# Kernel tuning notes

Hardware: AMD Instinct MI355X
Metric: run time of the kernel (lower is better)

## Reference

```python
import jax, jax.numpy as jnp
import numpy as np

N_NATIVE = 4_000_000
N_EDGES = 500_001  # -> 500_000 wl_centers
MAX_P = 15
TWO_PI = 2 * 3.1415926654  # constant as written in the torch source


def setup_inputs() -> dict:
    key = jax.random.key(0)
    k1, k2 = jax.random.split(key)

    # static wavelength grids (numpy, computed once)
    wl_native = np.linspace(9999.0, 10501.0, N_NATIVE)
    wl_bin_edges = np.linspace(10000.0, 10500.0, N_EDGES)

    # ragged segment labels: which data bin each native point falls into
    labels_np = np.searchsorted(wl_bin_edges, wl_native)  # values in [0, N_EDGES]
    num_segments = N_EDGES + 1
    counts_np = np.bincount(labels_np, minlength=num_segments).astype(np.float32)
    counts_np = np.maximum(counts_np, 1.0)  # all segments occupied by construction

    # polynomial design matrix over normalized bin centers
    wl_centers = 0.5 * (wl_bin_edges[1:] + wl_bin_edges[:-1])
    median_wl = np.median(wl_centers)
    bandwidth = wl_bin_edges[-1] + wl_bin_edges[0]
    wl_normed = (wl_centers - median_wl) / bandwidth
    design_np = wl_normed[:, None] ** np.arange(1, MAX_P + 1)[None, :]  # [500000, 15]

    kernel_grid_np = np.arange(-4.5, 4.51, 0.01)  # 901 taps

    return {
        "high_res_model": jax.random.uniform(k1, (N_NATIVE,), dtype=jnp.float32),
        "ln_sigma": jnp.asarray(-2.8134, dtype=jnp.float32),
        "weight": 0.01 * jax.random.normal(k2, (1, MAX_P), dtype=jnp.float32),
        "bias": jnp.ones((1,), dtype=jnp.float32),
        "kernel_grid": jnp.asarray(kernel_grid_np, dtype=jnp.float32),
        "design_matrix": jnp.asarray(design_np, dtype=jnp.float32),
        "labels": jnp.asarray(labels_np, dtype=jnp.int32),
        "counts": jnp.asarray(counts_np, dtype=jnp.float32),
    }


def reference(high_res_model, ln_sigma, weight, bias, kernel_grid, design_matrix, labels, counts):
    # --- instrumental_broaden: Gaussian conv1d, padding='same' ---
    sigma = 0.01 + jnp.exp(ln_sigma)
    gauss = (1.0 / (sigma * jnp.sqrt(jnp.asarray(TWO_PI, dtype=sigma.dtype)))) \
            * jnp.exp(-0.5 * kernel_grid ** 2 / sigma ** 2) * 0.01  # [901]
    # torch conv1d is cross-correlation; flip kernel for jnp.convolve (symmetric anyway)
    convolved = jnp.convolve(high_res_model, gauss[::-1], mode="same")  # [N_NATIVE]

    # --- resample_to_data: segment mean over ragged label groups ---
    num_segments = counts.shape[0]
    seg_sum = jax.ops.segment_sum(convolved, labels, num_segments=num_segments)
    seg_mean = seg_sum / counts
    resampled = jnp.clip(seg_mean, 0.0, 1.0)[1:-1]  # drop under/overflow bins -> [500000]

    # --- warped_continuum: linear model over polynomial design matrix ---
    continuum = design_matrix @ weight[0] + bias[0]  # [500000]

    return resampled * continuum
```

## Files before the change

### kernel.cpp

```cpp
#include <hip/hip_runtime.h>

#define BLOCK 256
#define SEGS  224
#define DN    2976
#define CVP   2112
#define SG_N  920
#define GTHR  1e-4f
#define NITF  14
#define NL4F  528

__device__ __forceinline__ double vnat(int i, double h, int N) {
    if (i == N - 1) return 10501.0;
    return __dadd_rn(__dmul_rn((double)i, h), 9999.0);
}

__device__ __forceinline__ int seg_start(int e, double h, double q, int N) {
    double E = (e >= 500000) ? 10500.0
                             : __dadd_rn(__dmul_rn((double)e, q), 10000.0);
    double g = (E - 9999.0) / h;
    int i = (int)g - 2;
    if (i < 0) i = 0;
    if (i > N) i = N;
    while (i < N && vnat(i, h, N) <= E) ++i;
    while (i > 0 && vnat(i - 1, h, N) > E) --i;
    return i;
}

__device__ __forceinline__ float continuum(int o, const float* __restrict__ wt,
                                           float bias0) {
    double eo  = 10000.0 + (double)o * 0.001;
    double eo1 = 10000.0 + (double)(o + 1) * 0.001;
    double ci  = 0.5 * (eo + eo1);
    double cA  = 0.5 * ((10000.0 + 249999.0 * 0.001) + (10000.0 + 250000.0 * 0.001));
    double cB  = 0.5 * ((10000.0 + 250000.0 * 0.001) + (10000.0 + 250001.0 * 0.001));
    double med = 0.5 * (cA + cB);
    float x = (float)((ci - med) / 20500.0);
    float c = bias0;
    float p = x;
    #pragma unroll
    for (int q = 0; q < 15; ++q) {
        c = fmaf(wt[q], p, c);
        p *= x;
    }
    return c;
}

__device__ __forceinline__ int swz(int p) { return p ^ ((p >> 3) & 1); }

__global__ __launch_bounds__(BLOCK) void fused_kernel(
        const float* __restrict__ a,
        const float* __restrict__ ln_sigma,
        const float* __restrict__ weight,
        const float* __restrict__ bias,
        float* __restrict__ out,
        int N, int M) {
    __shared__ __align__(16) float d[DN];
    __shared__ __align__(16) float sg[SG_N];
    __shared__ float cvp[CVP];
    __shared__ int aseg[256];

    const int t  = threadIdx.x;
    const int b  = blockIdx.x;
    const int o1 = b * SEGS + t;
    const int s0 = b * SEGS + 1;

    const double h = 502.0 / 3999999.0;
    const double q = 500.0 / 500000.0;

    const float sigma  = 0.01f + __expf(ln_sigma[0]);
    const float amp    = 0.01f / (sigma * sqrtf(6.2831853308f));
    const float inv2s2 = 0.5f / (sigma * sigma);
    int r = 450;
    float tg = amp / GTHR;
    if (tg > 1.0f) {
        float xstar = sigma * sqrtf(2.0f * __logf(tg));
        r = (int)(xstar * 100.0f) + 2;
        if (r > 450) r = 450;
    }

    const int Bblk  = seg_start(s0 - 1, h, q, N);
    const int gbase = (Bblk - 456) & ~3;
    const int off   = Bblk - 450 - gbase;
    int kLo = (450 - r) - ((450 - r + off) & 3);
    const int kHi   = 450 + r;
    const int nIter = (kHi - kLo + 4) >> 2;
    const int i40   = (off + kLo) >> 2;
    const bool fast = (nIter <= NITF);

    if (fast) {
        const int f0 = gbase + (i40 << 2);
        if (f0 >= 0 && f0 + (NL4F << 2) <= N) {
            const float4* A4 = reinterpret_cast<const float4*>(a) + (f0 >> 2);
            float4* dw = reinterpret_cast<float4*>(d);
            dw[swz(t)]       = A4[t];
            dw[swz(t + 256)] = A4[t + 256];
            if (t < NL4F - 512) dw[swz(t + 512)] = A4[t + 512];
        } else {
            for (int j = t; j < (NL4F << 2); j += BLOCK) {
                int gi = f0 + j;
                float v = (gi >= 0 && gi < N) ? a[gi] : 0.0f;
                d[(swz(j >> 2) << 2) | (j & 3)] = v;
            }
        }
        for (int j = t; j < 512; j += BLOCK) {
            const int k = j >> 6, i = j & 63;
            const int tap = kLo + i;
            float g = 0.0f;
            if (tap >= 0 && tap <= 900) {
                float x = (float)((tap - 450) * 0.01);
                g = amp * __expf(-x * x * inv2s2);
            }
            sg[68 * k + i] = g;
        }
    } else {
        int NL = off + 2016 + kHi + 6;
        if (NL > DN) NL = DN;
        const int NL4 = (NL + 3) >> 2;
        if (gbase >= 0 && gbase + (NL4 << 2) <= N) {
            const float4* a4 = reinterpret_cast<const float4*>(a) + (gbase >> 2);
            float4* dw = reinterpret_cast<float4*>(d);
            for (int j = t; j < NL4; j += BLOCK) dw[j] = a4[j];
        } else {
            for (int j = t; j < (NL4 << 2); j += BLOCK) {
                int gi = gbase + j;
                d[j] = (gi >= 0 && gi < N) ? a[gi] : 0.0f;
            }
        }
        const int ntap = (nIter << 2) + 8;
        for (int j = t; j < ntap; j += BLOCK) {
            int tap = kLo + j;
            float g = 0.0f;
            if (tap >= 0 && tap <= 900) {
                float x = (float)((tap - 450) * 0.01);
                g = amp * __expf(-x * x * inv2s2);
            }
            sg[j] = g;
        }
    }

    {
        int sc = s0 + t;
        if (sc > 500001) sc = 500001;
        aseg[t] = seg_start(sc - 1, h, q, N);
    }
    __syncthreads();

    const int A_t  = aseg[t];
    const int A_t1 = (t < 255) ? aseg[t + 1] : A_t;
    const int cnt  = (t < SEGS && o1 < M) ? (A_t1 - A_t) : 0;
    const int excl = A_t - Bblk;

    if (fast) {
        const float4* dr = reinterpret_cast<const float4*>(d);
        const float4* gr = reinterpret_cast<const float4*>(sg) + 17 * (t & 7);
        const int p0 = 2 * t;
        float4 W0 = dr[swz(p0)];
        float4 W1 = dr[swz(p0 + 1)];
        float c0=0.f,c1=0.f,c2=0.f,c3=0.f,c4=0.f,c5=0.f,c6=0.f,c7=0.f;
        #pragma unroll
        for (int m = 0; m < NITF; ++m) {
            const float4 W2 = dr[swz(p0 + m + 2)];
            const float4 g  = gr[m];
            c0 = fmaf(g.x, W0.x, c0); c0 = fmaf(g.y, W0.y, c0);
            c0 = fmaf(g.z, W0.z, c0); c0 = fmaf(g.w, W0.w, c0);
            c1 = fmaf(g.x, W0.y, c1); c1 = fmaf(g.y, W0.z, c1);
            c1 = fmaf(g.z, W0.w, c1); c1 = fmaf(g.w, W1.x, c1);
            c2 = fmaf(g.x, W0.z, c2); c2 = fmaf(g.y, W0.w, c2);
            c2 = fmaf(g.z, W1.x, c2); c2 = fmaf(g.w, W1.y, c2);
            c3 = fmaf(g.x, W0.w, c3); c3 = fmaf(g.y, W1.x, c3);
            c3 = fmaf(g.z, W1.y, c3); c3 = fmaf(g.w, W1.z, c3);
            c4 = fmaf(g.x, W1.x, c4); c4 = fmaf(g.y, W1.y, c4);
            c4 = fmaf(g.z, W1.z, c4); c4 = fmaf(g.w, W1.w, c4);
            c5 = fmaf(g.x, W1.y, c5); c5 = fmaf(g.y, W1.z, c5);
            c5 = fmaf(g.z, W1.w, c5); c5 = fmaf(g.w, W2.x, c5);
            c6 = fmaf(g.x, W1.z, c6); c6 = fmaf(g.y, W1.w, c6);
            c6 = fmaf(g.z, W2.x, c6); c6 = fmaf(g.w, W2.y, c6);
            c7 = fmaf(g.x, W1.w, c7); c7 = fmaf(g.y, W2.x, c7);
            c7 = fmaf(g.z, W2.y, c7); c7 = fmaf(g.w, W2.z, c7);
            W0 = W1; W1 = W2;
        }
        const int L = 8 * t;
        int j;
        j = L;     cvp[j + (j >> 5)] = c0;
        j = L + 1; cvp[j + (j >> 5)] = c1;
        j = L + 2; cvp[j + (j >> 5)] = c2;
        j = L + 3; cvp[j + (j >> 5)] = c3;
        j = L + 4; cvp[j + (j >> 5)] = c4;
        j = L + 5; cvp[j + (j >> 5)] = c5;
        j = L + 6; cvp[j + (j >> 5)] = c6;
        j = L + 7; cvp[j + (j >> 5)] = c7;
    } else {
        const float4* d4 = reinterpret_cast<const float4*>(d);
        const float4* s4 = reinterpret_cast<const float4*>(sg);
        const int ia = i40 + t, ib = ia + 256;
        float4 vA = d4[ia],     vB = d4[ib];
        float4 nA = d4[ia + 1], nB = d4[ib + 1];
        float4 gq = s4[0];
        float c0=0.f,c1=0.f,c2=0.f,c3=0.f,c4=0.f,c5=0.f,c6=0.f,c7=0.f;
        for (int m = 1; m <= nIter; ++m) {
            const float4 pA = d4[ia + m + 1];
            const float4 pB = d4[ib + m + 1];
            const float4 hq = s4[m];
            c0 = fmaf(gq.x, vA.x, c0); c0 = fmaf(gq.y, vA.y, c0);
            c0 = fmaf(gq.z, vA.z, c0); c0 = fmaf(gq.w, vA.w, c0);
            c1 = fmaf(gq.x, vA.y, c1); c1 = fmaf(gq.y, vA.z, c1);
            c1 = fmaf(gq.z, vA.w, c1); c1 = fmaf(gq.w, nA.x, c1);
            c2 = fmaf(gq.x, vA.z, c2); c2 = fmaf(gq.y, vA.w, c2);
            c2 = fmaf(gq.z, nA.x, c2); c2 = fmaf(gq.w, nA.y, c2);
            c3 = fmaf(gq.x, vA.w, c3); c3 = fmaf(gq.y, nA.x, c3);
            c3 = fmaf(gq.z, nA.y, c3); c3 = fmaf(gq.w, nA.z, c3);
            c4 = fmaf(gq.x, vB.x, c4); c4 = fmaf(gq.y, vB.y, c4);
            c4 = fmaf(gq.z, vB.z, c4); c4 = fmaf(gq.w, vB.w, c4);
            c5 = fmaf(gq.x, vB.y, c5); c5 = fmaf(gq.y, vB.z, c5);
            c5 = fmaf(gq.z, vB.w, c5); c5 = fmaf(gq.w, nB.x, c5);
            c6 = fmaf(gq.x, vB.z, c6); c6 = fmaf(gq.y, vB.w, c6);
            c6 = fmaf(gq.z, nB.x, c6); c6 = fmaf(gq.w, nB.y, c6);
            c7 = fmaf(gq.x, vB.w, c7); c7 = fmaf(gq.y, nB.x, c7);
            c7 = fmaf(gq.z, nB.y, c7); c7 = fmaf(gq.w, nB.z, c7);
            vA = nA; nA = pA; vB = nB; nB = pB; gq = hq;
        }
        const int La = 4 * t, Lb = 1024 + 4 * t;
        int j;
        j = La;     cvp[j + (j >> 5)] = c0;
        j = La + 1; cvp[j + (j >> 5)] = c1;
        j = La + 2; cvp[j + (j >> 5)] = c2;
        j = La + 3; cvp[j + (j >> 5)] = c3;
        j = Lb;     cvp[j + (j >> 5)] = c4;
        j = Lb + 1; cvp[j + (j >> 5)] = c5;
        j = Lb + 2; cvp[j + (j >> 5)] = c6;
        j = Lb + 3; cvp[j + (j >> 5)] = c7;
    }
    __syncthreads();

    if (t >= SEGS || o1 >= M) return;

    float sum = 0.0f;
    for (int i = 0; i < cnt; ++i) {
        int j = excl + i;
        sum += cvp[j + (j >> 5)];
    }
    float mean = fminf(fmaxf(sum / (float)cnt, 0.0f), 1.0f);
    out[o1] = mean * continuum(o1, weight, bias[0]);
}

extern "C" void kernel_launch(void* const* d_in, const int* in_sizes, int n_in,
                              void* d_out, int out_size, void* d_ws, size_t ws_size,
                              hipStream_t stream) {
    const float* a      = (const float*)d_in[0];
    const float* ln_s   = (const float*)d_in[1];
    const float* weight = (const float*)d_in[2];
    const float* bias   = (const float*)d_in[3];
    float* out = (float*)d_out;

    const int N = in_sizes[0];
    const int M = out_size;

    const int nb = (M + SEGS - 1) / SEGS;
    fused_kernel<<<nb, BLOCK, 0, stream>>>(a, ln_s, weight, bias, out, N, M);
}
```

Measured before the change: 19.53 us.

## Issue input tile load before segment search and pool shared memory for occupancy

The fast path now starts its global float4 load of the input window before the serial seg_start search. It estimates the window start arithmetically instead of waiting for the exact block boundary, so load latency overlaps with the double-precision search. Shared buffers are merged into one aliased pool and launch bounds request 8 blocks per SM to raise occupancy. Double divisions become reciprocal multiplies, and the slow path is replaced by a simple direct global-memory convolution. The slow path may be much slower when sigma is large, and the estimated window start may not cover every case.

```diff
diff --git a/kernel.cpp b/kernel.cpp
--- a/kernel.cpp
+++ b/kernel.cpp
@@ -2,22 +2,23 @@
 
 #define BLOCK 256
 #define SEGS  224
-#define DN    2976
-#define CVP   2112
-#define SG_N  920
 #define GTHR  1e-4f
 #define NITF  14
-#define NL4F  528
+#define NQ    534
+#define SG_F   2136
+#define CVP_F  2688
+#define ASEG_F 4800
+#define POOL_F 5056
 
 __device__ __forceinline__ double vnat(int i, double h, int N) {
     if (i == N - 1) return 10501.0;
     return __dadd_rn(__dmul_rn((double)i, h), 9999.0);
 }
 
-__device__ __forceinline__ int seg_start(int e, double h, double q, int N) {
+__device__ __forceinline__ int seg_start(int e, double h, double inv_h, int N) {
     double E = (e >= 500000) ? 10500.0
-                             : __dadd_rn(__dmul_rn((double)e, q), 10000.0);
-    double g = (E - 9999.0) / h;
+                             : __dadd_rn(__dmul_rn((double)e, 0.001), 10000.0);
+    double g = __dmul_rn(E - 9999.0, inv_h);
     int i = (int)g - 2;
     if (i < 0) i = 0;
     if (i > N) i = N;
@@ -34,7 +35,7 @@
     double cA  = 0.5 * ((10000.0 + 249999.0 * 0.001) + (10000.0 + 250000.0 * 0.001));
     double cB  = 0.5 * ((10000.0 + 250000.0 * 0.001) + (10000.0 + 250001.0 * 0.001));
     double med = 0.5 * (cA + cB);
-    float x = (float)((ci - med) / 20500.0);
+    float x = (float)((ci - med) * (1.0 / 20500.0));
     float c = bias0;
     float p = x;
     #pragma unroll
@@ -47,25 +48,27 @@
 
 __device__ __forceinline__ int swz(int p) { return p ^ ((p >> 3) & 1); }
 
-__global__ __launch_bounds__(BLOCK) void fused_kernel(
+__global__ __launch_bounds__(BLOCK, 8) void fused_kernel(
         const float* __restrict__ a,
         const float* __restrict__ ln_sigma,
         const float* __restrict__ weight,
         const float* __restrict__ bias,
         float* __restrict__ out,
         int N, int M) {
-    __shared__ __align__(16) float d[DN];
-    __shared__ __align__(16) float sg[SG_N];
-    __shared__ float cvp[CVP];
-    __shared__ int aseg[256];
+    __shared__ __align__(16) float pool[POOL_F];
+    float* dd   = pool;
+    float* sgf  = pool + SG_F;
+    float* sgs  = pool;
+    float* cvp  = pool + CVP_F;
+    int*   aseg = (int*)(pool + ASEG_F);
 
     const int t  = threadIdx.x;
     const int b  = blockIdx.x;
     const int o1 = b * SEGS + t;
     const int s0 = b * SEGS + 1;
 
-    const double h = 502.0 / 3999999.0;
-    const double q = 500.0 / 500000.0;
+    const double h     = 502.0 / 3999999.0;
+    const double inv_h = 3999999.0 / 502.0;
 
     const float sigma  = 0.01f + __expf(ln_sigma[0]);
     const float amp    = 0.01f / (sigma * sqrtf(6.2831853308f));
@@ -77,55 +80,44 @@
         r = (int)(xstar * 100.0f) + 2;
         if (r > 450) r = 450;
     }
-
-    const int Bblk  = seg_start(s0 - 1, h, q, N);
-    const int gbase = (Bblk - 456) & ~3;
-    const int off   = Bblk - 450 - gbase;
-    int kLo = (450 - r) - ((450 - r + off) & 3);
+    const bool fast = (r <= 26);
+
+    const int e0 = b * SEGS;
+    const double E0   = __dadd_rn(__dmul_rn((double)e0, 0.001), 10000.0);
+    const double iest = __dmul_rn(E0 - 9999.0, inv_h);
+    const int st0 = (((int)iest) - r - 16) & ~3;
+
+    if (fast) {
+        if (st0 >= 0 && st0 + (NQ << 2) <= N) {
+            const float4* A4 = reinterpret_cast<const float4*>(a) + (st0 >> 2);
+            float4* dw = reinterpret_cast<float4*>(dd);
+            dw[swz(t)]       = A4[t];
+            dw[swz(t + 256)] = A4[t + 256];
+            if (t < NQ - 512) dw[swz(t + 512)] = A4[t + 512];
+        } else {
+            for (int j = t; j < (NQ << 2); j += BLOCK) {
+                int gi = st0 + j;
+                float v = (gi >= 0 && gi < N) ? a[gi] : 0.0f;
+                dd[(swz(j >> 2) << 2) | (j & 3)] = v;
+            }
+        }
+    }
+
+    const int Bblk = seg_start(e0, h, inv_h, N);
+    const int off2 = Bblk - 450 - st0;
+    int kLo = (450 - r) - ((450 - r + off2) & 3);
     const int kHi   = 450 + r;
     const int nIter = (kHi - kLo + 4) >> 2;
-    const int i40   = (off + kLo) >> 2;
-    const bool fast = (nIter <= NITF);
+    const int i40   = (off2 + kLo) >> 2;
 
     if (fast) {
-        const int f0 = gbase + (i40 << 2);
-        if (f0 >= 0 && f0 + (NL4F << 2) <= N) {
-            const float4* A4 = reinterpret_cast<const float4*>(a) + (f0 >> 2);
-            float4* dw = reinterpret_cast<float4*>(d);
-            dw[swz(t)]       = A4[t];
-            dw[swz(t + 256)] = A4[t + 256];
-            if (t < NL4F - 512) dw[swz(t + 512)] = A4[t + 512];
-        } else {
-            for (int j = t; j < (NL4F << 2); j += BLOCK) {
-                int gi = f0 + j;
-                float v = (gi >= 0 && gi < N) ? a[gi] : 0.0f;
-                d[(swz(j >> 2) << 2) | (j & 3)] = v;
-            }
-        }
         for (int j = t; j < 512; j += BLOCK) {
             const int k = j >> 6, i = j & 63;
             const int tap = kLo + i;
-            float g = 0.0f;
-            if (tap >= 0 && tap <= 900) {
-                float x = (float)((tap - 450) * 0.01);
-                g = amp * __expf(-x * x * inv2s2);
-            }
-            sg[68 * k + i] = g;
+            float x = (float)((tap - 450) * 0.01);
+            sgf[68 * k + i] = amp * __expf(-x * x * inv2s2);
         }
     } else {
-        int NL = off + 2016 + kHi + 6;
-        if (NL > DN) NL = DN;
-        const int NL4 = (NL + 3) >> 2;
-        if (gbase >= 0 && gbase + (NL4 << 2) <= N) {
-            const float4* a4 = reinterpret_cast<const float4*>(a) + (gbase >> 2);
-            float4* dw = reinterpret_cast<float4*>(d);
-            for (int j = t; j < NL4; j += BLOCK) dw[j] = a4[j];
-        } else {
-            for (int j = t; j < (NL4 << 2); j += BLOCK) {
-                int gi = gbase + j;
-                d[j] = (gi >= 0 && gi < N) ? a[gi] : 0.0f;
-            }
-        }
         const int ntap = (nIter << 2) + 8;
         for (int j = t; j < ntap; j += BLOCK) {
             int tap = kLo + j;
@@ -134,14 +126,14 @@
                 float x = (float)((tap - 450) * 0.01);
                 g = amp * __expf(-x * x * inv2s2);
             }
-            sg[j] = g;
+            sgs[j] = g;
         }
     }
 
     {
         int sc = s0 + t;
         if (sc > 500001) sc = 500001;
-        aseg[t] = seg_start(sc - 1, h, q, N);
+        aseg[t] = seg_start(sc - 1, h, inv_h, N);
     }
     __syncthreads();
 
@@ -151,9 +143,9 @@
     const int excl = A_t - Bblk;
 
     if (fast) {
-        const float4* dr = reinterpret_cast<const float4*>(d);
-        const float4* gr = reinterpret_cast<const float4*>(sg) + 17 * (t & 7);
-        const int p0 = 2 * t;
+        const float4* dr = reinterpret_cast<const float4*>(dd);
+        const float4* gr = reinterpret_cast<const float4*>(sgf) + 17 * (t & 7);
+        const int p0 = i40 + 2 * t;
         float4 W0 = dr[swz(p0)];
         float4 W1 = dr[swz(p0 + 1)];
         float c0=0.f,c1=0.f,c2=0.f,c3=0.f,c4=0.f,c5=0.f,c6=0.f,c7=0.f;
@@ -190,45 +182,18 @@
         j = L + 6; cvp[j + (j >> 5)] = c6;
         j = L + 7; cvp[j + (j >> 5)] = c7;
     } else {
-        const float4* d4 = reinterpret_cast<const float4*>(d);
-        const float4* s4 = reinterpret_cast<const float4*>(sg);
-        const int ia = i40 + t, ib = ia + 256;
-        float4 vA = d4[ia],     vB = d4[ib];
-        float4 nA = d4[ia + 1], nB = d4[ib + 1];
-        float4 gq = s4[0];
-        float c0=0.f,c1=0.f,c2=0.f,c3=0.f,c4=0.f,c5=0.f,c6=0.f,c7=0.f;
-        for (int m = 1; m <= nIter; ++m) {
-            const float4 pA = d4[ia + m + 1];
-            const float4 pB = d4[ib + m + 1];
-            const float4 hq = s4[m];
-            c0 = fmaf(gq.x, vA.x, c0); c0 = fmaf(gq.y, vA.y, c0);
-            c0 = fmaf(gq.z, vA.z, c0); c0 = fmaf(gq.w, vA.w, c0);
-            c1 = fmaf(gq.x, vA.y, c1); c1 = fmaf(gq.y, vA.z, c1);
-            c1 = fmaf(gq.z, vA.w, c1); c1 = fmaf(gq.w, nA.x, c1);
-            c2 = fmaf(gq.x, vA.z, c2); c2 = fmaf(gq.y, vA.w, c2);
-            c2 = fmaf(gq.z, nA.x, c2); c2 = fmaf(gq.w, nA.y, c2);
-            c3 = fmaf(gq.x, vA.w, c3); c3 = fmaf(gq.y, nA.x, c3);
-            c3 = fmaf(gq.z, nA.y, c3); c3 = fmaf(gq.w, nA.z, c3);
-            c4 = fmaf(gq.x, vB.x, c4); c4 = fmaf(gq.y, vB.y, c4);
-            c4 = fmaf(gq.z, vB.z, c4); c4 = fmaf(gq.w, vB.w, c4);
-            c5 = fmaf(gq.x, vB.y, c5); c5 = fmaf(gq.y, vB.z, c5);
-            c5 = fmaf(gq.z, vB.w, c5); c5 = fmaf(gq.w, nB.x, c5);
-            c6 = fmaf(gq.x, vB.z, c6); c6 = fmaf(gq.y, vB.w, c6);
-            c6 = fmaf(gq.z, nB.x, c6); c6 = fmaf(gq.w, nB.y, c6);
-            c7 = fmaf(gq.x, vB.w, c7); c7 = fmaf(gq.y, nB.x, c7);
-            c7 = fmaf(gq.z, nB.y, c7); c7 = fmaf(gq.w, nB.z, c7);
-            vA = nA; nA = pA; vB = nB; nB = pB; gq = hq;
-        }
-        const int La = 4 * t, Lb = 1024 + 4 * t;
-        int j;
-        j = La;     cvp[j + (j >> 5)] = c0;
-        j = La + 1; cvp[j + (j >> 5)] = c1;
-        j = La + 2; cvp[j + (j >> 5)] = c2;
-        j = La + 3; cvp[j + (j >> 5)] = c3;
-        j = Lb;     cvp[j + (j >> 5)] = c4;
-        j = Lb + 1; cvp[j + (j >> 5)] = c5;
-        j = Lb + 2; cvp[j + (j >> 5)] = c6;
-        j = Lb + 3; cvp[j + (j >> 5)] = c7;
+        #pragma unroll 1
+        for (int u = 0; u < 8; ++u) {
+            const int p = Bblk + 8 * t + u;
+            float s = 0.0f;
+            for (int k = kLo; k <= kHi; ++k) {
+                const int gi = p + k - 450;
+                const float av = (gi >= 0 && gi < N) ? a[gi] : 0.0f;
+                s = fmaf(av, sgs[k - kLo], s);
+            }
+            const int j = 8 * t + u;
+            cvp[j + (j >> 5)] = s;
+        }
     }
     __syncthreads();
 
```

Result: faster. 18.39 us (-5.8%).
